# Optimization experiments

Measured on AMD Instinct MI355X. Metric: run time of the kernel, lower is better.

Reference implementation:

```python
import jax, jax.numpy as jnp
import numpy as np

D = 2048
B, L = 4, 4096

def log_g(x):
    # where(x>=0, log(relu(x)+0.5), -softplus(-x))
    return jnp.where(x >= 0, jnp.log(jax.nn.relu(x) + 0.5), -jax.nn.softplus(-x))

def setup_inputs() -> dict:
    key = jax.random.key(0)
    kx, kz, kn = jax.random.split(key, 3)
    x = jax.random.normal(kx, (B, L, D), dtype=jnp.float32)
    # kaiming_normal for Linear(D, D): std = sqrt(2 / fan_in)
    std = np.sqrt(2.0 / D).astype(np.float32)
    Wz = jax.random.normal(kz, (D, D), dtype=jnp.float32) * std
    Wn = jax.random.normal(kn, (D, D), dtype=jnp.float32) * std
    bz = jnp.zeros((D,), dtype=jnp.float32)
    bn = jnp.zeros((D,), dtype=jnp.float32)
    return {"x": x, "Wz": Wz, "bz": bz, "Wn": Wn, "bn": bn}

def reference(x, Wz, bz, Wn, bn):
    Bq, Lq, Dq = x.shape
    k = jnp.einsum('bld,ed->ble', x, Wz) + bz          # fc_z(x)
    log_z = -jax.nn.softplus(-k)                        # log sigmoid(k)
    log_coeffs = -jax.nn.softplus(k)                    # log(1 - sigmoid(k))
    log_h0 = jnp.full((Bq, 1, Dq), jnp.log(0.5), dtype=x.dtype)  # log_g(0)
    log_h_ = log_g(jnp.einsum('bld,ed->ble', x, Wn) + bn)        # log_g(fc_n(x))
    log_values = jnp.concatenate([log_h0, log_z + log_h_], axis=1)   # (B, L+1, D)
    a_star = jnp.pad(jnp.cumsum(log_coeffs, axis=1), ((0, 0), (1, 0), (0, 0)))  # (B, L+1, D)
    log_h = a_star + jax.lax.cumlogsumexp(log_values - a_star, axis=1)
    return jnp.exp(log_h)[:, 1:]
```

## Files before the change

### kernel.cpp

```cpp
#include <hip/hip_runtime.h>
#include <hip/hip_bf16.h>


#define D_DIM 2048
#define B_DIM 4
#define L_DIM 4096
#define M_DIM (B_DIM * L_DIM)
#define KDIM  D_DIM
#define NT    (KDIM / 64)
#define CHUNK 64
#define NCHUNK (L_DIM / CHUNK)

typedef __bf16 bf16x8 __attribute__((ext_vector_type(8)));
typedef float  f32x4  __attribute__((ext_vector_type(4)));

__device__ __forceinline__ unsigned short f2bf(float f) {
  unsigned int u = __float_as_uint(f);
  u += 0x7FFFu + ((u >> 16) & 1u);
  return (unsigned short)(u >> 16);
}
__device__ __forceinline__ float bf2f(unsigned short s) {
  return __uint_as_float(((unsigned int)s) << 16);
}

__device__ __forceinline__ void load_lds16(const void* g, void* l) {
  __builtin_amdgcn_global_load_lds(
      (const __attribute__((address_space(1))) void*)g,
      (__attribute__((address_space(3))) void*)l, 16, 0, 0);
}

__global__ __launch_bounds__(256) void cast_inputs(
    const float* __restrict__ x, const float* __restrict__ Wz,
    const float* __restrict__ Wn,
    unsigned short* __restrict__ xb, unsigned short* __restrict__ wb) {
  const size_t MK4 = (size_t)M_DIM * KDIM / 4;
  const size_t DD4 = (size_t)D_DIM * D_DIM / 4;
  size_t i = (size_t)blockIdx.x * 256 + threadIdx.x;
  const float4* src; ushort4* dst; size_t off;
  if (i < MK4)            { src = (const float4*)x;  dst = (ushort4*)xb; off = i; }
  else if (i < MK4 + DD4) { src = (const float4*)Wz; dst = (ushort4*)wb; off = i - MK4; }
  else                    { src = (const float4*)Wn;
                            dst = (ushort4*)(wb + (size_t)D_DIM * D_DIM);
                            off = i - MK4 - DD4; }
  float4 v = src[off];
  ushort4 o;
  o.x = f2bf(v.x); o.y = f2bf(v.y); o.z = f2bf(v.z); o.w = f2bf(v.w);
  dst[off] = o;
}

__global__ __launch_bounds__(512, 2) void gemm_fused(
    const unsigned short* __restrict__ xb, const unsigned short* __restrict__ wb,
    const float* __restrict__ bzv, const float* __restrict__ bnv,
    unsigned short* __restrict__ Ab, unsigned short* __restrict__ Gb) {
  __shared__ unsigned short lds[2][4][8192];
  const int t = threadIdx.x;
  const int lane = t & 63;
  const int wid = t >> 6;
  const int wm = wid >> 2, wn = wid & 3;
  const int laneRow = lane & 15, lg = lane >> 4;

  const int bid = blockIdx.x;
  const int swz = (bid & 7) * 128 + (bid >> 3);
  const int mtile = swz >> 4;
  const int ntile = swz & 15;

  const unsigned short* aBase = xb + (size_t)mtile * 256 * KDIM;
  const unsigned short* bBase = wb + (size_t)ntile * 256 * KDIM;

  const int r0 = t >> 3;
  const int sSwz = (t & 7) ^ (r0 & 7);

#define STAGE(buf, reg, srcB, halfRow, kt) do {                                   \
    const unsigned short* s_ = (srcB) + (size_t)((halfRow) + r0) * KDIM           \
                               + (kt) * 64 + sSwz * 8;                            \
    unsigned short* d_ = &lds[buf][reg][t * 8];                                   \
    load_lds16(s_, d_);                                                           \
    load_lds16(s_ + 64 * KDIM, d_ + 4096);                                        \
  } while (0)

  const int sA0 = ((0 + lg) ^ (laneRow & 7)) * 8;
  const int sA1 = ((4 + lg) ^ (laneRow & 7)) * 8;
  const int bRow0 = (wn & 1) * 64;

  f32x4 acc[8][4] = {};

  STAGE(0, 2, bBase, 0, 0);  STAGE(0, 3, bBase, 128, 0);
  STAGE(0, 0, aBase, 0, 0);  STAGE(0, 1, aBase, 128, 0);
  STAGE(1, 2, bBase, 0, 1);  STAGE(1, 3, bBase, 128, 1);
  asm volatile("s_waitcnt vmcnt(4)" ::: "memory");
  __builtin_amdgcn_sched_barrier(0);
  __builtin_amdgcn_s_barrier();

#define MFMA_QUAD(qm, qn)                                                         \
  _Pragma("unroll") for (int m = 0; m < 4; ++m)                                   \
  _Pragma("unroll") for (int n = 0; n < 2; ++n)                                   \
  _Pragma("unroll") for (int k = 0; k < 2; ++k)                                   \
    acc[(qm)*4 + m][(qn)*2 + n] = __builtin_amdgcn_mfma_f32_16x16x32_bf16(        \
        aF[m*2 + k], bF[((qn)*2 + n)*2 + k], acc[(qm)*4 + m][(qn)*2 + n], 0, 0, 0)

  for (int U = 0; U < NT; ++U) {
    const int cur = U & 1;
    const unsigned short* ldsA = lds[cur][wm];
    const unsigned short* ldsB = lds[cur][2 + (wn >> 1)];
    bf16x8 aF[8], bF[8];

#pragma unroll
    for (int m = 0; m < 4; ++m) {
      aF[m*2+0] = *(const bf16x8*)&ldsA[(m*16 + laneRow) * 64 + sA0];
      aF[m*2+1] = *(const bf16x8*)&ldsA[(m*16 + laneRow) * 64 + sA1];
    }
#pragma unroll
    for (int n = 0; n < 2; ++n) {
      bF[n*2+0] = *(const bf16x8*)&ldsB[(bRow0 + n*16 + laneRow) * 64 + sA0];
      bF[n*2+1] = *(const bf16x8*)&ldsB[(bRow0 + n*16 + laneRow) * 64 + sA1];
    }
    if (U + 1 < NT) STAGE(cur ^ 1, 0, aBase, 0, U + 1);
    __builtin_amdgcn_s_barrier();
    __builtin_amdgcn_s_setprio(1);
    MFMA_QUAD(0, 0);
    __builtin_amdgcn_s_setprio(0);
    __builtin_amdgcn_s_barrier();

#pragma unroll
    for (int n = 0; n < 2; ++n) {
      bF[4 + n*2+0] = *(const bf16x8*)&ldsB[(bRow0 + 32 + n*16 + laneRow) * 64 + sA0];
      bF[4 + n*2+1] = *(const bf16x8*)&ldsB[(bRow0 + 32 + n*16 + laneRow) * 64 + sA1];
    }
    if (U + 1 < NT) STAGE(cur ^ 1, 1, aBase, 128, U + 1);
    __builtin_amdgcn_s_barrier();
    __builtin_amdgcn_s_setprio(1);
    MFMA_QUAD(0, 1);
    __builtin_amdgcn_s_setprio(0);
    __builtin_amdgcn_s_barrier();

#pragma unroll
    for (int m = 0; m < 4; ++m) {
      aF[m*2+0] = *(const bf16x8*)&ldsA[(64 + m*16 + laneRow) * 64 + sA0];
      aF[m*2+1] = *(const bf16x8*)&ldsA[(64 + m*16 + laneRow) * 64 + sA1];
    }
    if (U + 2 < NT) STAGE(cur, 2, bBase, 0, U + 2);
    __builtin_amdgcn_s_barrier();
    __builtin_amdgcn_s_setprio(1);
    MFMA_QUAD(1, 0);
    __builtin_amdgcn_s_setprio(0);
    __builtin_amdgcn_s_barrier();

    if (U + 2 < NT) {
      STAGE(cur, 3, bBase, 128, U + 2);
      asm volatile("s_waitcnt vmcnt(4)" ::: "memory");
      __builtin_amdgcn_sched_barrier(0);
    } else if (U + 1 < NT) {
      asm volatile("s_waitcnt vmcnt(0)" ::: "memory");
      __builtin_amdgcn_sched_barrier(0);
    }
    __builtin_amdgcn_s_barrier();
    __builtin_amdgcn_s_setprio(1);
    MFMA_QUAD(1, 1);
    __builtin_amdgcn_s_setprio(0);
    __builtin_amdgcn_s_barrier();
  }

  const int gcB = ntile * 256 + wn * 64;
  const int grB = mtile * 256 + wm * 128;
  const bool isZ = (ntile < 8);
  unsigned short* outP = isZ ? Ab : Gb;
  float bias[4];
#pragma unroll
  for (int ni = 0; ni < 4; ++ni) {
    const int gc = gcB + ni * 16 + laneRow;
    bias[ni] = isZ ? bzv[gc] : bnv[gc - D_DIM];
  }
#pragma unroll
  for (int mi = 0; mi < 8; ++mi) {
#pragma unroll
    for (int ni = 0; ni < 4; ++ni) {
      const int gc = gcB + ni * 16 + laneRow;
      const int dcol = isZ ? gc : gc - D_DIM;
#pragma unroll
      for (int j = 0; j < 4; ++j) {
        const float val = acc[mi][ni][j] + bias[ni];
        const int gr = grB + mi * 16 + (lg << 2) + j;
        const size_t off = (size_t)gr * D_DIM + dcol;
        if (isZ) outP[off] = f2bf(1.0f / (1.0f + __expf(val)));
        else     outP[off] = f2bf(val >= 0.0f ? val + 0.5f
                                              : 1.0f / (1.0f + __expf(-val)));
      }
    }
  }
#undef STAGE
#undef MFMA_QUAD
}

__global__ __launch_bounds__(256) void scan_pass1(
    const unsigned short* __restrict__ Ab, const unsigned short* __restrict__ Gb,
    float* __restrict__ SA, float* __restrict__ SV) {
  const int tid = blockIdx.x * 256 + threadIdx.x;
  const int dp = tid & 1023;
  const int c = (tid >> 10) & (NCHUNK - 1);
  const int b = tid >> 16;
  const unsigned int* A32 = (const unsigned int*)Ab;
  const unsigned int* G32 = (const unsigned int*)Gb;
  size_t basePair = ((size_t)b * L_DIM + (size_t)c * CHUNK) * 1024 + dp;
  float A0 = 1.0f, V0 = 0.0f, A1 = 1.0f, V1 = 0.0f;
#pragma unroll 8
  for (int i = 0; i < CHUNK; ++i) {
    unsigned int av = A32[basePair + (size_t)i * 1024];
    unsigned int gv = G32[basePair + (size_t)i * 1024];
    float a0 = __uint_as_float(av << 16), a1 = __uint_as_float(av & 0xFFFF0000u);
    float g0 = __uint_as_float(gv << 16), g1 = __uint_as_float(gv & 0xFFFF0000u);
    V0 = a0 * V0 + (1.0f - a0) * g0;  A0 *= a0;
    V1 = a1 * V1 + (1.0f - a1) * g1;  A1 *= a1;
  }
  const size_t sidx = ((size_t)b * NCHUNK + c) * D_DIM + (size_t)dp * 2;
  *(float2*)&SA[sidx] = make_float2(A0, A1);
  *(float2*)&SV[sidx] = make_float2(V0, V1);
}

__global__ __launch_bounds__(256) void scan_pass2(
    const float* __restrict__ SA, const float* __restrict__ SV,
    float* __restrict__ H0) {
  const int tid = blockIdx.x * 256 + threadIdx.x;
  const int d = tid & (D_DIM - 1);
  const int b = tid >> 11;
  float h = 0.5f;
  for (int c = 0; c < NCHUNK; ++c) {
    size_t idx = ((size_t)b * NCHUNK + c) * D_DIM + d;
    H0[idx] = h;
    h = SA[idx] * h + SV[idx];
  }
}

__global__ __launch_bounds__(256) void scan_pass3(
    const unsigned short* __restrict__ Ab, const unsigned short* __restrict__ Gb,
    const float* __restrict__ H0, float* __restrict__ out) {
  const int tid = blockIdx.x * 256 + threadIdx.x;
  const int dp = tid & 1023;
  const int c = (tid >> 10) & (NCHUNK - 1);
  const int b = tid >> 16;
  const unsigned int* A32 = (const unsigned int*)Ab;
  const unsigned int* G32 = (const unsigned int*)Gb;
  size_t basePair = ((size_t)b * L_DIM + (size_t)c * CHUNK) * 1024 + dp;
  const size_t hidx = ((size_t)b * NCHUNK + c) * D_DIM + (size_t)dp * 2;
  float2 h2 = *(const float2*)&H0[hidx];
  float h0 = h2.x, h1 = h2.y;
#pragma unroll 8
  for (int i = 0; i < CHUNK; ++i) {
    unsigned int av = A32[basePair + (size_t)i * 1024];
    unsigned int gv = G32[basePair + (size_t)i * 1024];
    float a0 = __uint_as_float(av << 16), a1 = __uint_as_float(av & 0xFFFF0000u);
    float g0 = __uint_as_float(gv << 16), g1 = __uint_as_float(gv & 0xFFFF0000u);
    h0 = a0 * h0 + (1.0f - a0) * g0;
    h1 = a1 * h1 + (1.0f - a1) * g1;
    *(float2*)&out[(basePair + (size_t)i * 1024) * 2] = make_float2(h0, h1);
  }
}

extern "C" void kernel_launch(void* const* d_in, const int* in_sizes, int n_in,
                              void* d_out, int out_size, void* d_ws, size_t ws_size,
                              hipStream_t stream) {
  const float* x  = (const float*)d_in[0];
  const float* Wz = (const float*)d_in[1];
  const float* bz = (const float*)d_in[2];
  const float* Wn = (const float*)d_in[3];
  const float* bn = (const float*)d_in[4];
  float* out = (float*)d_out;

  char* ws = (char*)d_ws;
  unsigned short* xb = (unsigned short*)(ws);
  unsigned short* wb = (unsigned short*)(ws + 67108864);
  unsigned short* Ab = (unsigned short*)(ws + 83886080);
  unsigned short* Gb = (unsigned short*)(ws + 150994944);
  float* SA = (float*)(ws + 218103808);
  float* SV = (float*)(ws + 220200960);
  float* H0 = (float*)(ws + 222298112);

  cast_inputs<<<40960, 256, 0, stream>>>(x, Wz, Wn, xb, wb);
  gemm_fused<<<1024, 512, 0, stream>>>(xb, wb, bz, bn, Ab, Gb);
  scan_pass1<<<1024, 256, 0, stream>>>(Ab, Gb, SA, SV);
  scan_pass2<<<32, 256, 0, stream>>>(SA, SV, H0);
  scan_pass3<<<1024, 256, 0, stream>>>(Ab, Gb, H0, out);
}
```

Measured before the change: 576.6 us.

## Prefetch GEMM A tiles two stages ahead and vectorize scan to four channels

In the GEMM main loop, the A-tile loads for step U+2 now go into the current buffer at the end of each iteration, once all A fragments have been read into registers. Previously the A tile for U+1 was staged mid-iteration. This deepens the A prefetch distance to match B, with more loads in flight (vmcnt 8). Separately, both scan passes now handle four channels per thread using 8-byte bf16 loads and 16-byte output stores, with half as many blocks. This gives wider memory transactions but fewer threads to hide memory latency.

```diff
diff --git a/kernel.cpp b/kernel.cpp
--- a/kernel.cpp
+++ b/kernel.cpp
@@ -19,8 +19,11 @@
   u += 0x7FFFu + ((u >> 16) & 1u);
   return (unsigned short)(u >> 16);
 }
-__device__ __forceinline__ float bf2f(unsigned short s) {
-  return __uint_as_float(((unsigned int)s) << 16);
+__device__ __forceinline__ float bflo(unsigned int u) {
+  return __uint_as_float(u << 16);
+}
+__device__ __forceinline__ float bfhi(unsigned int u) {
+  return __uint_as_float(u & 0xFFFF0000u);
 }
 
 __device__ __forceinline__ void load_lds16(const void* g, void* l) {
@@ -87,7 +90,8 @@
   STAGE(0, 2, bBase, 0, 0);  STAGE(0, 3, bBase, 128, 0);
   STAGE(0, 0, aBase, 0, 0);  STAGE(0, 1, aBase, 128, 0);
   STAGE(1, 2, bBase, 0, 1);  STAGE(1, 3, bBase, 128, 1);
-  asm volatile("s_waitcnt vmcnt(4)" ::: "memory");
+  STAGE(1, 0, aBase, 0, 1);  STAGE(1, 1, aBase, 128, 1);
+  asm volatile("s_waitcnt vmcnt(8)" ::: "memory");
   __builtin_amdgcn_sched_barrier(0);
   __builtin_amdgcn_s_barrier();
 
@@ -114,7 +118,6 @@
       bF[n*2+0] = *(const bf16x8*)&ldsB[(bRow0 + n*16 + laneRow) * 64 + sA0];
       bF[n*2+1] = *(const bf16x8*)&ldsB[(bRow0 + n*16 + laneRow) * 64 + sA1];
     }
-    if (U + 1 < NT) STAGE(cur ^ 1, 0, aBase, 0, U + 1);
     __builtin_amdgcn_s_barrier();
     __builtin_amdgcn_s_setprio(1);
     MFMA_QUAD(0, 0);
@@ -126,7 +129,6 @@
       bF[4 + n*2+0] = *(const bf16x8*)&ldsB[(bRow0 + 32 + n*16 + laneRow) * 64 + sA0];
       bF[4 + n*2+1] = *(const bf16x8*)&ldsB[(bRow0 + 32 + n*16 + laneRow) * 64 + sA1];
     }
-    if (U + 1 < NT) STAGE(cur ^ 1, 1, aBase, 128, U + 1);
     __builtin_amdgcn_s_barrier();
     __builtin_amdgcn_s_setprio(1);
     MFMA_QUAD(0, 1);
@@ -147,7 +149,9 @@
 
     if (U + 2 < NT) {
       STAGE(cur, 3, bBase, 128, U + 2);
-      asm volatile("s_waitcnt vmcnt(4)" ::: "memory");
+      STAGE(cur, 0, aBase, 0, U + 2);
+      STAGE(cur, 1, aBase, 128, U + 2);
+      asm volatile("s_waitcnt vmcnt(8)" ::: "memory");
       __builtin_amdgcn_sched_barrier(0);
     } else if (U + 1 < NT) {
       asm volatile("s_waitcnt vmcnt(0)" ::: "memory");
@@ -195,25 +199,28 @@
     const unsigned short* __restrict__ Ab, const unsigned short* __restrict__ Gb,
     float* __restrict__ SA, float* __restrict__ SV) {
   const int tid = blockIdx.x * 256 + threadIdx.x;
-  const int dp = tid & 1023;
-  const int c = (tid >> 10) & (NCHUNK - 1);
-  const int b = tid >> 16;
-  const unsigned int* A32 = (const unsigned int*)Ab;
-  const unsigned int* G32 = (const unsigned int*)Gb;
-  size_t basePair = ((size_t)b * L_DIM + (size_t)c * CHUNK) * 1024 + dp;
-  float A0 = 1.0f, V0 = 0.0f, A1 = 1.0f, V1 = 0.0f;
+  const int dq = tid & 511;
+  const int c = (tid >> 9) & (NCHUNK - 1);
+  const int b = tid >> 15;
+  const uint2* A2 = (const uint2*)Ab;
+  const uint2* G2 = (const uint2*)Gb;
+  size_t base = ((size_t)b * L_DIM + (size_t)c * CHUNK) * 512 + dq;
+  float A0 = 1.0f, A1 = 1.0f, A2r = 1.0f, A3 = 1.0f;
+  float V0 = 0.0f, V1 = 0.0f, V2 = 0.0f, V3 = 0.0f;
 #pragma unroll 8
   for (int i = 0; i < CHUNK; ++i) {
-    unsigned int av = A32[basePair + (size_t)i * 1024];
-    unsigned int gv = G32[basePair + (size_t)i * 1024];
-    float a0 = __uint_as_float(av << 16), a1 = __uint_as_float(av & 0xFFFF0000u);
-    float g0 = __uint_as_float(gv << 16), g1 = __uint_as_float(gv & 0xFFFF0000u);
+    uint2 av = A2[base + (size_t)i * 512];
+    uint2 gv = G2[base + (size_t)i * 512];
+    float a0 = bflo(av.x), a1 = bfhi(av.x), a2 = bflo(av.y), a3 = bfhi(av.y);
+    float g0 = bflo(gv.x), g1 = bfhi(gv.x), g2 = bflo(gv.y), g3 = bfhi(gv.y);
     V0 = a0 * V0 + (1.0f - a0) * g0;  A0 *= a0;
     V1 = a1 * V1 + (1.0f - a1) * g1;  A1 *= a1;
-  }
-  const size_t sidx = ((size_t)b * NCHUNK + c) * D_DIM + (size_t)dp * 2;
-  *(float2*)&SA[sidx] = make_float2(A0, A1);
-  *(float2*)&SV[sidx] = make_float2(V0, V1);
+    V2 = a2 * V2 + (1.0f - a2) * g2;  A2r *= a2;
+    V3 = a3 * V3 + (1.0f - a3) * g3;  A3 *= a3;
+  }
+  const size_t sidx = ((size_t)b * NCHUNK + c) * D_DIM + (size_t)dq * 4;
+  *(float4*)&SA[sidx] = make_float4(A0, A1, A2r, A3);
+  *(float4*)&SV[sidx] = make_float4(V0, V1, V2, V3);
 }
 
 __global__ __launch_bounds__(256) void scan_pass2(
@@ -234,24 +241,27 @@
     const unsigned short* __restrict__ Ab, const unsigned short* __restrict__ Gb,
     const float* __restrict__ H0, float* __restrict__ out) {
   const int tid = blockIdx.x * 256 + threadIdx.x;
-  const int dp = tid & 1023;
-  const int c = (tid >> 10) & (NCHUNK - 1);
-  const int b = tid >> 16;
-  const unsigned int* A32 = (const unsigned int*)Ab;
-  const unsigned int* G32 = (const unsigned int*)Gb;
-  size_t basePair = ((size_t)b * L_DIM + (size_t)c * CHUNK) * 1024 + dp;
-  const size_t hidx = ((size_t)b * NCHUNK + c) * D_DIM + (size_t)dp * 2;
-  float2 h2 = *(const float2*)&H0[hidx];
-  float h0 = h2.x, h1 = h2.y;
+  const int dq = tid & 511;
+  const int c = (tid >> 9) & (NCHUNK - 1);
+  const int b = tid >> 15;
+  const uint2* A2 = (const uint2*)Ab;
+  const uint2* G2 = (const uint2*)Gb;
+  size_t base = ((size_t)b * L_DIM + (size_t)c * CHUNK) * 512 + dq;
+  const size_t hidx = ((size_t)b * NCHUNK + c) * D_DIM + (size_t)dq * 4;
+  float4 h4 = *(const float4*)&H0[hidx];
+  float h0 = h4.x, h1 = h4.y, h2 = h4.z, h3 = h4.w;
+  float4* out4 = (float4*)out;
 #pragma unroll 8
   for (int i = 0; i < CHUNK; ++i) {
-    unsigned int av = A32[basePair + (size_t)i * 1024];
-    unsigned int gv = G32[basePair + (size_t)i * 1024];
-    float a0 = __uint_as_float(av << 16), a1 = __uint_as_float(av & 0xFFFF0000u);
-    float g0 = __uint_as_float(gv << 16), g1 = __uint_as_float(gv & 0xFFFF0000u);
+    uint2 av = A2[base + (size_t)i * 512];
+    uint2 gv = G2[base + (size_t)i * 512];
+    float a0 = bflo(av.x), a1 = bfhi(av.x), a2 = bflo(av.y), a3 = bfhi(av.y);
+    float g0 = bflo(gv.x), g1 = bfhi(gv.x), g2 = bflo(gv.y), g3 = bfhi(gv.y);
     h0 = a0 * h0 + (1.0f - a0) * g0;
     h1 = a1 * h1 + (1.0f - a1) * g1;
-    *(float2*)&out[(basePair + (size_t)i * 1024) * 2] = make_float2(h0, h1);
+    h2 = a2 * h2 + (1.0f - a2) * g2;
+    h3 = a3 * h3 + (1.0f - a3) * g3;
+    out4[base + (size_t)i * 512] = make_float4(h0, h1, h2, h3);
   }
 }
 
@@ -276,7 +286,7 @@
 
   cast_inputs<<<40960, 256, 0, stream>>>(x, Wz, Wn, xb, wb);
   gemm_fused<<<1024, 512, 0, stream>>>(xb, wb, bz, bn, Ab, Gb);
-  scan_pass1<<<1024, 256, 0, stream>>>(Ab, Gb, SA, SV);
+  scan_pass1<<<512, 256, 0, stream>>>(Ab, Gb, SA, SV);
   scan_pass2<<<32, 256, 0, stream>>>(SA, SV, H0);
-  scan_pass3<<<1024, 256, 0, stream>>>(Ab, Gb, H0, out);
-}
+  scan_pass3<<<512, 256, 0, stream>>>(Ab, Gb, H0, out);
+}
```

Result: no change. 587.8 us (+1.9%).
